# Optimization experiments

Measured on AMD Instinct MI355X. Metric: run time of the kernel, lower is better.

## Reference

```python
import jax, jax.numpy as jnp
import numpy as np

N_NODES = 20000; N_EDGES = 320000; B = 128; T = 200
EMB = 128; GH = 64; HEADS = 4; LH = 128; NSP = 64; TD = 4

def gat_conv(x, src, dst, W, att_src, att_dst, bias, heads, ch, concat):
    # PyG GATConv (eval mode, dropout off): per-edge attention + segment softmax over dst
    n = x.shape[0]
    h = (x @ W).reshape(n, heads, ch)                      # [N,H,C]
    a_s = (h * att_src[None]).sum(-1)                      # [N,H]
    a_d = (h * att_dst[None]).sum(-1)
    e = jax.nn.leaky_relu(a_s[src] + a_d[dst], 0.2)        # [E,H]
    e_max = jax.ops.segment_max(e, dst, num_segments=n)    # every node has a self-loop -> finite
    ex = jnp.exp(e - e_max[dst])
    denom = jax.ops.segment_sum(ex, dst, num_segments=n)
    alpha = ex / denom[dst]                                # [E,H]
    out = jax.ops.segment_sum(h[src] * alpha[:, :, None], dst, num_segments=n)  # [N,H,C]
    out = out.reshape(n, heads * ch) if concat else out.mean(axis=1)
    return out + bias

def lstm_dir(x, w_ih, w_hh, b):
    # single-direction LSTM, torch gate order (i, f, g, o)
    bsz = x.shape[0]
    def step(carry, xt):
        hprev, cprev = carry
        g = xt @ w_ih.T + hprev @ w_hh.T + b
        i, f, gg, o = jnp.split(g, 4, axis=-1)
        c = jax.nn.sigmoid(f) * cprev + jax.nn.sigmoid(i) * jnp.tanh(gg)
        hnew = jax.nn.sigmoid(o) * jnp.tanh(c)
        return (hnew, c), hnew
    init = (jnp.zeros((bsz, LH), x.dtype), jnp.zeros((bsz, LH), x.dtype))
    _, hs = jax.lax.scan(step, init, jnp.swapaxes(x, 0, 1))
    return jnp.swapaxes(hs, 0, 1)

def forward(x_coords, temporal_features, node_emb,
            gat1_W, gat1_att_src, gat1_att_dst, gat1_bias,
            gat2_W, gat2_att_src, gat2_att_dst, gat2_bias,
            w_ih_f, w_hh_f, b_f, w_ih_b, w_hh_b, b_b,
            attn_node_w, attn_node_b, attn_sp_w, attn_sp_b,
            fc_node_W, fc_node_b, fc_sp_W, fc_sp_b,
            edge_index, seq, lengths):
    n = x_coords.shape[0]
    node_features = jnp.concatenate([x_coords, node_emb, temporal_features], axis=1)  # [N,134]
    loops = jnp.arange(n)                                  # PyG GATConv add_self_loops=True
    src = jnp.concatenate([edge_index[0], loops])
    dst = jnp.concatenate([edge_index[1], loops])
    z = jax.nn.elu(gat_conv(node_features, src, dst, gat1_W, gat1_att_src, gat1_att_dst, gat1_bias, HEADS, GH, True))
    z = gat_conv(z, src, dst, gat2_W, gat2_att_src, gat2_att_dst, gat2_bias, 1, EMB, False)
    seq_emb = z[seq]                                       # [B,T,EMB]
    out_f = lstm_dir(seq_emb, w_ih_f, w_hh_f, b_f)
    # backward direction of packed BiLSTM: reverse each sequence within its true length
    rev_idx = jnp.clip(lengths[:, None] - 1 - jnp.arange(T)[None, :], 0, T - 1)
    x_rev = jnp.take_along_axis(seq_emb, rev_idx[:, :, None], axis=1)
    out_b = jnp.take_along_axis(lstm_dir(x_rev, w_ih_b, w_hh_b, b_b), rev_idx[:, :, None], axis=1)
    lstm_out = jnp.concatenate([out_f, out_b], axis=-1)    # [B,T,2*LH]
    mask = jnp.arange(T)[None, :] < lengths[:, None]
    def attnpool(w, bias):
        scores = jnp.where(mask, lstm_out @ w + bias, -jnp.inf)
        aw = jax.nn.softmax(scores, axis=1)
        return jnp.einsum('bt,bth->bh', aw, lstm_out)
    ctx_n = attnpool(attn_node_w, attn_node_b)
    ctx_s = attnpool(attn_sp_w, attn_sp_b)
    return (ctx_n @ fc_node_W + fc_node_b, ctx_s @ fc_sp_W + fc_sp_b)

def setup_inputs() -> dict:
    key = jax.random.key(0)
    ks = jax.random.split(key, 24)
    f = lambda i, shape, s=0.05: jax.random.normal(ks[i], shape, jnp.float32) * s
    return dict(
        x_coords=f(0, (N_NODES, 2), 1.0),
        temporal_features=f(1, (N_NODES, TD), 1.0),
        node_emb=f(2, (N_NODES, EMB)),
        gat1_W=f(3, (2 + EMB + TD, HEADS * GH)),
        gat1_att_src=f(4, (HEADS, GH)),
        gat1_att_dst=f(5, (HEADS, GH)),
        gat1_bias=jnp.zeros((HEADS * GH,), jnp.float32),
        gat2_W=f(6, (HEADS * GH, EMB)),
        gat2_att_src=f(7, (1, EMB)),
        gat2_att_dst=f(8, (1, EMB)),
        gat2_bias=jnp.zeros((EMB,), jnp.float32),
        w_ih_f=f(9, (4 * LH, EMB)), w_hh_f=f(10, (4 * LH, LH)), b_f=jnp.zeros((4 * LH,), jnp.float32),
        w_ih_b=f(11, (4 * LH, EMB)), w_hh_b=f(12, (4 * LH, LH)), b_b=jnp.zeros((4 * LH,), jnp.float32),
        attn_node_w=f(13, (2 * LH,)), attn_node_b=jnp.zeros((1,), jnp.float32),
        attn_sp_w=f(14, (2 * LH,)), attn_sp_b=jnp.zeros((1,), jnp.float32),
        fc_node_W=f(15, (2 * LH, N_NODES)), fc_node_b=jnp.zeros((N_NODES,), jnp.float32),
        fc_sp_W=f(16, (2 * LH, NSP)), fc_sp_b=jnp.zeros((NSP,), jnp.float32),
        edge_index=jax.random.randint(ks[17], (2, N_EDGES), 0, N_NODES),
        seq=jax.random.randint(ks[18], (B, T), 0, N_NODES),
        lengths=jax.random.randint(ks[19], (B,), 1, T + 1),
    )

def reference(x_coords, temporal_features, node_emb,
              gat1_W, gat1_att_src, gat1_att_dst, gat1_bias,
              gat2_W, gat2_att_src, gat2_att_dst, gat2_bias,
              w_ih_f, w_hh_f, b_f, w_ih_b, w_hh_b, b_b,
              attn_node_w, attn_node_b, attn_sp_w, attn_sp_b,
              fc_node_W, fc_node_b, fc_sp_W, fc_sp_b,
              edge_index, seq, lengths):
    return forward(x_coords, temporal_features, node_emb,
                   gat1_W, gat1_att_src, gat1_att_dst, gat1_bias,
                   gat2_W, gat2_att_src, gat2_att_dst, gat2_bias,
                   w_ih_f, w_hh_f, b_f, w_ih_b, w_hh_b, b_b,
                   attn_node_w, attn_node_b, attn_sp_w, attn_sp_b,
                   fc_node_W, fc_node_b, fc_sp_W, fc_sp_b,
                   edge_index, seq, lengths)
```

## Files before the change

### kernel.cpp

```cpp
#include <hip/hip_runtime.h>
#include <cstdint>
#include <cstddef>

#define N_NODES 20000
#define N_EDGES 320000
#define NE_TOT  (N_EDGES + N_NODES)
#define BB 128
#define TT 200
#define EMB 128
#define GH 64
#define HEADS 4
#define LH 128
#define NSP 64
#define KF 136

__global__ void k_count(const int* __restrict__ ei, int* __restrict__ cnt) {
    int e = blockIdx.x * blockDim.x + threadIdx.x;
    if (e >= NE_TOT) return;
    int d = (e < N_EDGES) ? ei[N_EDGES + e] : (e - N_EDGES);
    atomicAdd(&cnt[d], 1);
}

__global__ __launch_bounds__(1024) void k_scan(const int* __restrict__ cnt, int* __restrict__ rs) {
    __shared__ int sd[1024];
    __shared__ int carry_s;
    int tid = threadIdx.x;
    if (tid == 0) carry_s = 0;
    __syncthreads();
    for (int base = 0; base < N_NODES; base += 1024) {
        int v = (base + tid < N_NODES) ? cnt[base + tid] : 0;
        int x = v;
        sd[tid] = x;
        __syncthreads();
        for (int off = 1; off < 1024; off <<= 1) {
            int t = (tid >= off) ? sd[tid - off] : 0;
            __syncthreads();
            x += t; sd[tid] = x;
            __syncthreads();
        }
        int carry = carry_s;
        if (base + tid < N_NODES) rs[base + tid] = carry + x - v;
        __syncthreads();
        if (tid == 0) carry_s = carry + sd[1023];
        __syncthreads();
    }
    if (tid == 0) rs[N_NODES] = carry_s;
}

__global__ void k_scatter(const int* __restrict__ ei, int* __restrict__ cursor, int* __restrict__ csr) {
    int e = blockIdx.x * blockDim.x + threadIdx.x;
    if (e >= NE_TOT) return;
    int s, d;
    if (e < N_EDGES) { s = ei[e]; d = ei[N_EDGES + e]; }
    else             { s = d = e - N_EDGES; }
    int pos = atomicAdd(&cursor[d], 1);
    csr[pos] = s;
}

__global__ void k_build_nf(const float* __restrict__ xc, const float* __restrict__ tf,
                           const float* __restrict__ ne, float* __restrict__ nf) {
    int n = blockIdx.x, j = threadIdx.x;
    if (j >= KF) return;
    float v = 0.f;
    if (j < 2)        v = xc[n * 2 + j];
    else if (j < 130) v = ne[n * 128 + (j - 2)];
    else if (j < 134) v = tf[n * 4 + (j - 130)];
    nf[(size_t)n * KF + j] = v;
}

__global__ void k_build_w1p(const float* __restrict__ W, float* __restrict__ Wp) {
    int k = blockIdx.x, n = threadIdx.x;
    Wp[k * 256 + n] = (k < 134) ? W[k * 256 + n] : 0.f;
}

__global__ void k_transpose_cat(const float* __restrict__ W, float* __restrict__ WT, int colOff) {
    int idx = blockIdx.x * blockDim.x + threadIdx.x;
    if (idx >= 512 * 128) return;
    int g = idx & 511, k = idx >> 9;
    WT[k * 1024 + colOff + g] = W[g * 128 + k];
}

__global__ void k_build_bcat(const float* __restrict__ bf, const float* __restrict__ bb,
                             float* __restrict__ bcat) {
    int t = threadIdx.x;
    bcat[t] = bf[t];
    bcat[512 + t] = bb[t];
}

__global__ void k_len_prefix(const int* __restrict__ lengths, int* __restrict__ loff) {
    if (threadIdx.x == 0) {
        int acc = 0;
        for (int b = 0; b < BB; b++) { loff[b] = acc; acc += lengths[b]; }
        loff[BB] = acc;
    }
}

__global__ void k_build_rowmap(const int* __restrict__ lengths, const int* __restrict__ loff,
                               const int* __restrict__ seq, int* __restrict__ rowsrc,
                               int* __restrict__ rowdst) {
    int idx = blockIdx.x * blockDim.x + threadIdx.x;
    if (idx >= BB * TT) return;
    int b = idx / TT, t = idx - b * TT;
    if (t >= lengths[b]) return;
    int pos = loff[b] + t;
    rowsrc[pos] = seq[idx];
    rowdst[pos] = idx;
}

__global__ __launch_bounds__(256) void k_gemm_f32(
    const float* __restrict__ A, const float* __restrict__ B, float* __restrict__ C,
    int M, int N, int K, const int* __restrict__ gather, const float* __restrict__ bias)
{
    __shared__ float As[8][68];
    __shared__ float Bs[8][68];
    int tid = threadIdx.x;
    int bm = blockIdx.y << 6, bn = blockIdx.x << 6;
    int tm = (tid >> 4) << 2, tn = (tid & 15) << 2;
    float acc[4][4] = {};
    for (int k0 = 0; k0 < K; k0 += 8) {
        if (tid < 128) {
            int m = tid >> 1, kq = (tid & 1) << 2;
            int gm = bm + m;
            float4 v = make_float4(0.f, 0.f, 0.f, 0.f);
            if (gm < M) {
                int row = gather ? gather[gm] : gm;
                v = *(const float4*)(A + (size_t)row * K + k0 + kq);
            }
            As[kq + 0][m] = v.x; As[kq + 1][m] = v.y;
            As[kq + 2][m] = v.z; As[kq + 3][m] = v.w;
        } else {
            int t2 = tid - 128;
            int kk = t2 >> 4, n4 = (t2 & 15) << 2;
            int gn = bn + n4;
            float4 v = make_float4(0.f, 0.f, 0.f, 0.f);
            const float* brow = B + (size_t)(k0 + kk) * N;
            if (gn + 3 < N) v = *(const float4*)(brow + gn);
            else {
                if (gn + 0 < N) v.x = brow[gn + 0];
                if (gn + 1 < N) v.y = brow[gn + 1];
                if (gn + 2 < N) v.z = brow[gn + 2];
                if (gn + 3 < N) v.w = brow[gn + 3];
            }
            *(float4*)(&Bs[kk][n4]) = v;
        }
        __syncthreads();
#pragma unroll
        for (int k = 0; k < 8; k++) {
            float4 av = *(const float4*)&As[k][tm];
            float4 bv = *(const float4*)&Bs[k][tn];
            acc[0][0] += av.x * bv.x; acc[0][1] += av.x * bv.y; acc[0][2] += av.x * bv.z; acc[0][3] += av.x * bv.w;
            acc[1][0] += av.y * bv.x; acc[1][1] += av.y * bv.y; acc[1][2] += av.y * bv.z; acc[1][3] += av.y * bv.w;
            acc[2][0] += av.z * bv.x; acc[2][1] += av.z * bv.y; acc[2][2] += av.z * bv.z; acc[2][3] += av.z * bv.w;
            acc[3][0] += av.w * bv.x; acc[3][1] += av.w * bv.y; acc[3][2] += av.w * bv.z; acc[3][3] += av.w * bv.w;
        }
        __syncthreads();
    }
#pragma unroll
    for (int i = 0; i < 4; i++) {
        int gm = bm + tm + i;
        if (gm >= M) continue;
#pragma unroll
        for (int j = 0; j < 4; j++) {
            int gn = bn + tn + j;
            if (gn >= N) continue;
            float r = acc[i][j];
            if (bias) r += bias[gn];
            C[(size_t)gm * N + gn] = r;
        }
    }
}

__global__ __launch_bounds__(256) void k_gemm_f32_rs(
    const float* __restrict__ A, const float* __restrict__ B, float* __restrict__ C,
    const int* __restrict__ Mdev, int N, int K,
    const int* __restrict__ rowsrc, const int* __restrict__ rowdst,
    const float* __restrict__ bias)
{
    int M = Mdev[BB];
    int bm = blockIdx.y << 6, bn = blockIdx.x << 6;
    if (bm >= M) return;
    __shared__ float As[8][68];
    __shared__ float Bs[8][68];
    int tid = threadIdx.x;
    int tm = (tid >> 4) << 2, tn = (tid & 15) << 2;
    float acc[4][4] = {};
    for (int k0 = 0; k0 < K; k0 += 8) {
        if (tid < 128) {
            int m = tid >> 1, kq = (tid & 1) << 2;
            int gm = bm + m;
            float4 v = make_float4(0.f, 0.f, 0.f, 0.f);
            if (gm < M) {
                int row = rowsrc[gm];
                v = *(const float4*)(A + (size_t)row * K + k0 + kq);
            }
            As[kq + 0][m] = v.x; As[kq + 1][m] = v.y;
            As[kq + 2][m] = v.z; As[kq + 3][m] = v.w;
        } else {
            int t2 = tid - 128;
            int kk = t2 >> 4, n4 = (t2 & 15) << 2;
            int gn = bn + n4;
            const float* brow = B + (size_t)(k0 + kk) * N;
            *(float4*)(&Bs[kk][n4]) = *(const float4*)(brow + gn);
        }
        __syncthreads();
#pragma unroll
        for (int k = 0; k < 8; k++) {
            float4 av = *(const float4*)&As[k][tm];
            float4 bv = *(const float4*)&Bs[k][tn];
            acc[0][0] += av.x * bv.x; acc[0][1] += av.x * bv.y; acc[0][2] += av.x * bv.z; acc[0][3] += av.x * bv.w;
            acc[1][0] += av.y * bv.x; acc[1][1] += av.y * bv.y; acc[1][2] += av.y * bv.z; acc[1][3] += av.y * bv.w;
            acc[2][0] += av.z * bv.x; acc[2][1] += av.z * bv.y; acc[2][2] += av.z * bv.z; acc[2][3] += av.z * bv.w;
            acc[3][0] += av.w * bv.x; acc[3][1] += av.w * bv.y; acc[3][2] += av.w * bv.z; acc[3][3] += av.w * bv.w;
        }
        __syncthreads();
    }
#pragma unroll
    for (int i = 0; i < 4; i++) {
        int gm = bm + tm + i;
        if (gm >= M) continue;
        size_t crow = (size_t)rowdst[gm] * N;
#pragma unroll
        for (int j = 0; j < 4; j++) {
            int gn = bn + tn + j;
            float r = acc[i][j] + bias[gn];
            C[crow + gn] = r;
        }
    }
}

template <int H, int C>
__global__ void k_attn_dots(const float* __restrict__ hm, const float* __restrict__ asrc,
                            const float* __restrict__ adst, float* __restrict__ a_s,
                            float* __restrict__ a_d) {
    int wave = (blockIdx.x * blockDim.x + threadIdx.x) >> 6;
    int lane = threadIdx.x & 63;
    if (wave >= N_NODES * H) return;
    int n = wave / H, h = wave - n * H;
    const float* row = hm + (size_t)n * (H * C) + h * C;
    float ps = 0.f, pd = 0.f;
#pragma unroll
    for (int c0 = 0; c0 < C; c0 += 64) {
        float v = row[c0 + lane];
        ps += v * asrc[h * C + c0 + lane];
        pd += v * adst[h * C + c0 + lane];
    }
#pragma unroll
    for (int off = 32; off > 0; off >>= 1) {
        ps += __shfl_down(ps, off);
        pd += __shfl_down(pd, off);
    }
    if (lane == 0) { a_s[wave] = ps; a_d[wave] = pd; }
}

template <int H, int C, bool DO_ELU>
__global__ void k_gat_aggregate(const float* __restrict__ hm, const float* __restrict__ a_s,
                                const float* __restrict__ a_d, const int* __restrict__ rs,
                                const int* __restrict__ csr, const float* __restrict__ bias,
                                float* __restrict__ out) {
    int d = blockIdx.x;
    int tid = threadIdx.x;
    int h = tid / C;
    int r0 = rs[d], r1 = rs[d + 1];
    float adv = a_d[d * H + h];
    float m = -1e30f;
    for (int j = r0; j < r1; j++) {
        int s = csr[j];
        float e = a_s[s * H + h] + adv;
        e = (e > 0.f) ? e : 0.2f * e;
        m = fmaxf(m, e);
    }
    float den = 0.f, acc = 0.f;
    for (int j = r0; j < r1; j++) {
        int s = csr[j];
        float e = a_s[s * H + h] + adv;
        e = (e > 0.f) ? e : 0.2f * e;
        float ex = __expf(e - m);
        den += ex;
        acc += ex * hm[(size_t)s * (H * C) + tid];
    }
    float r = acc / den + bias[tid];
    if (DO_ELU) r = (r > 0.f) ? r : expm1f(r);
    out[(size_t)d * (H * C) + tid] = r;
}

__device__ __forceinline__ float sigmf(float x) { return 1.f / (1.f + __expf(-x)); }
__device__ __forceinline__ float tanhfast(float x) {
    x = fminf(fmaxf(x, -20.f), 20.f);
    float e = __expf(2.f * x);
    return (e - 1.f) / (e + 1.f);
}

__global__ __launch_bounds__(512, 2) void k_lstm(
    const float* __restrict__ xgcat,
    const float* __restrict__ whh_f, const float* __restrict__ whh_b,
    const int* __restrict__ lengths, float* __restrict__ lstm_out)
{
    int b = blockIdx.x & 127;
    int dir = blockIdx.x >> 7;
    int tid = threadIdx.x;
    int u = tid & 127;
    int j = tid >> 7;
    const float* whh = dir ? whh_b : whh_f;
    const float* xg = xgcat + (dir << 9);
    int L = lengths[b];
    float4 w4[4][8];
#pragma unroll
    for (int m = 0; m < 4; m++) {
        const float4* wrow = (const float4*)(whh + (size_t)(m * LH + u) * LH + j * 32);
#pragma unroll
        for (int q = 0; q < 8; q++) w4[m][q] = wrow[q];
    }
    __shared__ float hbuf[LH];
    __shared__ float pbuf[4][4 * LH];
    if (tid < LH) hbuf[tid] = 0.f;
    float c = 0.f;
    float hv = 0.f;
    float x0 = 0.f, x1 = 0.f, x2 = 0.f, x3 = 0.f;
    if (j == 0) {
        int tx0 = dir ? (L - 1) : 0;
        const float* xrow = xg + ((size_t)(b * TT + tx0) << 10);
        x0 = xrow[u]; x1 = xrow[LH + u]; x2 = xrow[2 * LH + u]; x3 = xrow[3 * LH + u];
    }
    __syncthreads();
    for (int t = 0; t < L; t++) {
        if (j == 0 && t > 0) {
            int txp = dir ? (L - t) : (t - 1);
            lstm_out[((size_t)b * TT + txp) * (2 * LH) + dir * LH + u] = hv;
        }
        float x0n = 0.f, x1n = 0.f, x2n = 0.f, x3n = 0.f;
        if (j == 0 && t + 1 < L) {
            int tx1 = dir ? (L - 2 - t) : (t + 1);
            const float* xrow = xg + ((size_t)(b * TT + tx1) << 10);
            x0n = xrow[u]; x1n = xrow[LH + u]; x2n = xrow[2 * LH + u]; x3n = xrow[3 * LH + u];
        }
        const float4* hp = (const float4*)(hbuf + j * 32);
        float4 h[8];
#pragma unroll
        for (int q = 0; q < 8; q++) h[q] = hp[q];
        float a0 = x0, a1 = x1, a2 = x2, a3 = x3;
#pragma unroll
        for (int q = 0; q < 8; q++) {
            float4 hq = h[q];
            a0 += w4[0][q].x * hq.x + w4[0][q].y * hq.y + w4[0][q].z * hq.z + w4[0][q].w * hq.w;
            a1 += w4[1][q].x * hq.x + w4[1][q].y * hq.y + w4[1][q].z * hq.z + w4[1][q].w * hq.w;
            a2 += w4[2][q].x * hq.x + w4[2][q].y * hq.y + w4[2][q].z * hq.z + w4[2][q].w * hq.w;
            a3 += w4[3][q].x * hq.x + w4[3][q].y * hq.y + w4[3][q].z * hq.z + w4[3][q].w * hq.w;
        }
        pbuf[j][0 * LH + u] = a0;
        pbuf[j][1 * LH + u] = a1;
        pbuf[j][2 * LH + u] = a2;
        pbuf[j][3 * LH + u] = a3;
        asm volatile("s_waitcnt lgkmcnt(0)" ::: "memory");
        __builtin_amdgcn_sched_barrier(0);
        __builtin_amdgcn_s_barrier();
        if (tid < LH) {
            float gi = (pbuf[0][0 * LH + u] + pbuf[1][0 * LH + u]) + (pbuf[2][0 * LH + u] + pbuf[3][0 * LH + u]);
            float gf = (pbuf[0][1 * LH + u] + pbuf[1][1 * LH + u]) + (pbuf[2][1 * LH + u] + pbuf[3][1 * LH + u]);
            float gG = (pbuf[0][2 * LH + u] + pbuf[1][2 * LH + u]) + (pbuf[2][2 * LH + u] + pbuf[3][2 * LH + u]);
            float go = (pbuf[0][3 * LH + u] + pbuf[1][3 * LH + u]) + (pbuf[2][3 * LH + u] + pbuf[3][3 * LH + u]);
            float ig = sigmf(gi);
            float fg = sigmf(gf);
            float gg = tanhfast(gG);
            float og = sigmf(go);
            c = fg * c + ig * gg;
            hv = og * tanhfast(c);
            hbuf[u] = hv;
        }
        asm volatile("s_waitcnt lgkmcnt(0)" ::: "memory");
        __builtin_amdgcn_sched_barrier(0);
        __builtin_amdgcn_s_barrier();
        x0 = x0n; x1 = x1n; x2 = x2n; x3 = x3n;
    }
    if (j == 0) {
        int txp = dir ? 0 : (L - 1);
        lstm_out[((size_t)b * TT + txp) * (2 * LH) + dir * LH + u] = hv;
    }
}

__global__ __launch_bounds__(256) void k_attnpool(
    const float* __restrict__ lo, const int* __restrict__ lengths,
    const float* __restrict__ wn, const float* __restrict__ bn,
    const float* __restrict__ wsp, const float* __restrict__ bsp,
    float* __restrict__ ctxn, float* __restrict__ ctxs)
{
    int b = blockIdx.x;
    int tid = threadIdx.x;
    int L = lengths[b];
    __shared__ float sn[TT], ss[TT];
    __shared__ float red[256];
    int wv = tid >> 6, lane = tid & 63;
    for (int t = wv; t < L; t += 4) {
        const float* row = lo + ((size_t)b * TT + t) * (2 * LH);
        float pn = 0.f, ps = 0.f;
#pragma unroll
        for (int c0 = 0; c0 < 256; c0 += 64) {
            float v = row[c0 + lane];
            pn += v * wn[c0 + lane];
            ps += v * wsp[c0 + lane];
        }
#pragma unroll
        for (int off = 32; off > 0; off >>= 1) {
            pn += __shfl_down(pn, off);
            ps += __shfl_down(ps, off);
        }
        if (lane == 0) { sn[t] = pn + bn[0]; ss[t] = ps + bsp[0]; }
    }
    __syncthreads();
    float vn = (tid < L) ? sn[tid] : -1e30f;
    float vs = (tid < L) ? ss[tid] : -1e30f;
    red[tid] = vn; __syncthreads();
    for (int s = 128; s > 0; s >>= 1) { if (tid < s) red[tid] = fmaxf(red[tid], red[tid + s]); __syncthreads(); }
    float mn = red[0]; __syncthreads();
    red[tid] = vs; __syncthreads();
    for (int s = 128; s > 0; s >>= 1) { if (tid < s) red[tid] = fmaxf(red[tid], red[tid + s]); __syncthreads(); }
    float ms = red[0]; __syncthreads();
    float en = (tid < L) ? __expf(vn - mn) : 0.f;
    float es = (tid < L) ? __expf(vs - ms) : 0.f;
    red[tid] = en; __syncthreads();
    for (int s = 128; s > 0; s >>= 1) { if (tid < s) red[tid] += red[tid + s]; __syncthreads(); }
    float dn = red[0]; __syncthreads();
    red[tid] = es; __syncthreads();
    for (int s = 128; s > 0; s >>= 1) { if (tid < s) red[tid] += red[tid + s]; __syncthreads(); }
    float dsum = red[0]; __syncthreads();
    if (tid < L) { sn[tid] = en / dn; ss[tid] = es / dsum; }
    __syncthreads();
    float an = 0.f, asv = 0.f;
    for (int t = 0; t < L; t++) {
        float v = lo[((size_t)b * TT + t) * (2 * LH) + tid];
        an += sn[t] * v;
        asv += ss[t] * v;
    }
    ctxn[b * (2 * LH) + tid] = an;
    ctxs[b * (2 * LH) + tid] = asv;
}

extern "C" void kernel_launch(void* const* d_in, const int* in_sizes, int n_in,
                              void* d_out, int out_size, void* d_ws, size_t ws_size,
                              hipStream_t stream) {
    (void)in_sizes; (void)n_in; (void)out_size; (void)ws_size;
    const float* x_coords = (const float*)d_in[0];
    const float* temporal = (const float*)d_in[1];
    const float* node_emb = (const float*)d_in[2];
    const float* gat1_W   = (const float*)d_in[3];
    const float* gat1_as  = (const float*)d_in[4];
    const float* gat1_ad  = (const float*)d_in[5];
    const float* gat1_b   = (const float*)d_in[6];
    const float* gat2_W   = (const float*)d_in[7];
    const float* gat2_as  = (const float*)d_in[8];
    const float* gat2_ad  = (const float*)d_in[9];
    const float* gat2_b   = (const float*)d_in[10];
    const float* w_ih_f   = (const float*)d_in[11];
    const float* w_hh_f   = (const float*)d_in[12];
    const float* b_f      = (const float*)d_in[13];
    const float* w_ih_b   = (const float*)d_in[14];
    const float* w_hh_b   = (const float*)d_in[15];
    const float* b_b      = (const float*)d_in[16];
    const float* attn_n_w = (const float*)d_in[17];
    const float* attn_n_b = (const float*)d_in[18];
    const float* attn_s_w = (const float*)d_in[19];
    const float* attn_s_b = (const float*)d_in[20];
    const float* fc_n_W   = (const float*)d_in[21];
    const float* fc_n_b   = (const float*)d_in[22];
    const float* fc_s_W   = (const float*)d_in[23];
    const float* fc_s_b   = (const float*)d_in[24];
    const int*   edge_idx = (const int*)d_in[25];
    const int*   seq      = (const int*)d_in[26];
    const int*   lengths  = (const int*)d_in[27];

    char* ws = (char*)d_ws;
    size_t off = 0;
    auto alloc = [&](size_t bytes) -> char* {
        char* p = ws + off;
        off += (bytes + 255) & ~(size_t)255;
        return p;
    };
    int*   cnt      = (int*)alloc((size_t)N_NODES * 4);
    int*   rowstart = (int*)alloc((size_t)(N_NODES + 1) * 4);
    int*   cursor   = (int*)alloc((size_t)N_NODES * 4);
    int*   csr      = (int*)alloc((size_t)NE_TOT * 4);
    float* z2       = (float*)alloc((size_t)N_NODES * EMB * 4);
    float* lstm_o   = (float*)alloc((size_t)BB * TT * 2 * LH * 4);
    float* ctxn     = (float*)alloc((size_t)BB * 2 * LH * 4);
    float* ctxs     = (float*)alloc((size_t)BB * 2 * LH * 4);
    float* wTcat    = (float*)alloc((size_t)128 * 1024 * 4);
    float* bcat     = (float*)alloc((size_t)1024 * 4);
    int*   loff     = (int*)alloc((size_t)(BB + 1) * 4);
    int*   rowsrc   = (int*)alloc((size_t)BB * TT * 4);
    int*   rowdst   = (int*)alloc((size_t)BB * TT * 4);
    float* nf  = (float*)(ws + off);
    float* w1p = nf + (size_t)N_NODES * KF;
    float* h1  = w1p + (size_t)KF * 256;
    float* as1 = h1 + (size_t)N_NODES * 256;
    float* ad1 = as1 + (size_t)N_NODES * 4;
    float* z1  = ad1 + (size_t)N_NODES * 4;
    float* h2  = z1 + (size_t)N_NODES * 256;
    float* as2 = h2 + (size_t)N_NODES * 128;
    float* ad2 = as2 + (size_t)N_NODES;
    float* xgcat = (float*)(ws + off);

    hipMemsetAsync(cnt, 0, (size_t)N_NODES * 4, stream);
    k_count<<<(NE_TOT + 255) / 256, 256, 0, stream>>>(edge_idx, cnt);
    k_scan<<<1, 1024, 0, stream>>>(cnt, rowstart);
    hipMemcpyAsync(cursor, rowstart, (size_t)N_NODES * 4, hipMemcpyDeviceToDevice, stream);
    k_scatter<<<(NE_TOT + 255) / 256, 256, 0, stream>>>(edge_idx, cursor, csr);

    k_len_prefix<<<1, 64, 0, stream>>>(lengths, loff);
    k_build_rowmap<<<(BB * TT + 255) / 256, 256, 0, stream>>>(lengths, loff, seq, rowsrc, rowdst);

    k_build_nf<<<N_NODES, 192, 0, stream>>>(x_coords, temporal, node_emb, nf);
    k_build_w1p<<<KF, 256, 0, stream>>>(gat1_W, w1p);
    {
        dim3 g(4, (N_NODES + 63) / 64);
        k_gemm_f32<<<g, 256, 0, stream>>>(nf, w1p, h1, N_NODES, 256, KF, nullptr, nullptr);
    }
    k_attn_dots<HEADS, GH><<<(N_NODES * HEADS + 3) / 4, 256, 0, stream>>>(h1, gat1_as, gat1_ad, as1, ad1);
    k_gat_aggregate<HEADS, GH, true><<<N_NODES, 256, 0, stream>>>(h1, as1, ad1, rowstart, csr, gat1_b, z1);

    {
        dim3 g(2, (N_NODES + 63) / 64);
        k_gemm_f32<<<g, 256, 0, stream>>>(z1, gat2_W, h2, N_NODES, 128, 256, nullptr, nullptr);
    }
    k_attn_dots<1, EMB><<<(N_NODES + 3) / 4, 256, 0, stream>>>(h2, gat2_as, gat2_ad, as2, ad2);
    k_gat_aggregate<1, EMB, false><<<N_NODES, 128, 0, stream>>>(h2, as2, ad2, rowstart, csr, gat2_b, z2);

    k_transpose_cat<<<(512 * 128 + 255) / 256, 256, 0, stream>>>(w_ih_f, wTcat, 0);
    k_transpose_cat<<<(512 * 128 + 255) / 256, 256, 0, stream>>>(w_ih_b, wTcat, 512);
    k_build_bcat<<<1, 512, 0, stream>>>(b_f, b_b, bcat);
    {
        dim3 g(1024 / 64, (BB * TT + 63) / 64);
        k_gemm_f32_rs<<<g, 256, 0, stream>>>(z2, wTcat, xgcat, loff, 1024, 128, rowsrc, rowdst, bcat);
    }

    k_lstm<<<256, 512, 0, stream>>>(xgcat, w_hh_f, w_hh_b, lengths, lstm_o);

    k_attnpool<<<BB, 256, 0, stream>>>(lstm_o, lengths, attn_n_w, attn_n_b, attn_s_w, attn_s_b, ctxn, ctxs);

    float* out_node = (float*)d_out;
    float* out_sp   = out_node + (size_t)BB * N_NODES;
    {
        dim3 g((N_NODES + 63) / 64, 2);
        k_gemm_f32<<<g, 256, 0, stream>>>(ctxn, fc_n_W, out_node, BB, N_NODES, 256, nullptr, fc_n_b);
    }
    {
        dim3 g(1, 2);
        k_gemm_f32<<<g, 256, 0, stream>>>(ctxs, fc_s_W, out_sp, BB, NSP, 256, nullptr, fc_s_b);
    }
}
```

Before: 791.5 us.

## Reduce LSTM gate partial sums with DPP lane shuffles and double-buffer hidden state

Result: no change. 800.6 us (+1.2%).

```diff
diff --git a/kernel.cpp b/kernel.cpp
--- a/kernel.cpp
+++ b/kernel.cpp
@@ -290,6 +290,15 @@
     return (e - 1.f) / (e + 1.f);
 }
 
+__device__ __forceinline__ float dpp_add_x1(float x) {
+    int y = __builtin_amdgcn_update_dpp(0, __float_as_int(x), 0xB1, 0xF, 0xF, true);
+    return x + __int_as_float(y);
+}
+__device__ __forceinline__ float dpp_add_x2(float x) {
+    int y = __builtin_amdgcn_update_dpp(0, __float_as_int(x), 0x4E, 0xF, 0xF, true);
+    return x + __int_as_float(y);
+}
+
 __global__ __launch_bounds__(512, 2) void k_lstm(
     const float* __restrict__ xgcat,
     const float* __restrict__ whh_f, const float* __restrict__ whh_b,
@@ -298,46 +307,48 @@
     int b = blockIdx.x & 127;
     int dir = blockIdx.x >> 7;
     int tid = threadIdx.x;
-    int u = tid & 127;
-    int j = tid >> 7;
+    int wv = tid >> 6;
+    int lane = tid & 63;
+    int kp = lane & 3;
+    int ul = lane >> 2;
+    int u = (wv << 4) + ul;
     const float* whh = dir ? whh_b : whh_f;
     const float* xg = xgcat + (dir << 9);
     int L = lengths[b];
     float4 w4[4][8];
 #pragma unroll
     for (int m = 0; m < 4; m++) {
-        const float4* wrow = (const float4*)(whh + (size_t)(m * LH + u) * LH + j * 32);
+        const float4* wrow = (const float4*)(whh + (size_t)(m * LH + u) * LH + kp * 32);
 #pragma unroll
         for (int q = 0; q < 8; q++) w4[m][q] = wrow[q];
     }
-    __shared__ float hbuf[LH];
-    __shared__ float pbuf[4][4 * LH];
-    if (tid < LH) hbuf[tid] = 0.f;
-    float c = 0.f;
-    float hv = 0.f;
+    __shared__ __align__(16) float hbuf[2][160];
+    if (tid < LH) hbuf[0][(tid >> 5) * 40 + (tid & 31)] = 0.f;
+    float c = 0.f, hv = 0.f;
+    const bool act = (kp == 0);
     float x0 = 0.f, x1 = 0.f, x2 = 0.f, x3 = 0.f;
-    if (j == 0) {
+    if (act) {
         int tx0 = dir ? (L - 1) : 0;
         const float* xrow = xg + ((size_t)(b * TT + tx0) << 10);
         x0 = xrow[u]; x1 = xrow[LH + u]; x2 = xrow[2 * LH + u]; x3 = xrow[3 * LH + u];
     }
     __syncthreads();
     for (int t = 0; t < L; t++) {
-        if (j == 0 && t > 0) {
+        if (act && t > 0) {
             int txp = dir ? (L - t) : (t - 1);
             lstm_out[((size_t)b * TT + txp) * (2 * LH) + dir * LH + u] = hv;
         }
         float x0n = 0.f, x1n = 0.f, x2n = 0.f, x3n = 0.f;
-        if (j == 0 && t + 1 < L) {
+        if (act && t + 1 < L) {
             int tx1 = dir ? (L - 2 - t) : (t + 1);
             const float* xrow = xg + ((size_t)(b * TT + tx1) << 10);
             x0n = xrow[u]; x1n = xrow[LH + u]; x2n = xrow[2 * LH + u]; x3n = xrow[3 * LH + u];
         }
-        const float4* hp = (const float4*)(hbuf + j * 32);
+        const float4* hp = (const float4*)(&hbuf[t & 1][kp * 40]);
         float4 h[8];
 #pragma unroll
         for (int q = 0; q < 8; q++) h[q] = hp[q];
-        float a0 = x0, a1 = x1, a2 = x2, a3 = x3;
+        float a0 = 0.f, a1 = 0.f, a2 = 0.f, a3 = 0.f;
 #pragma unroll
         for (int q = 0; q < 8; q++) {
             float4 hq = h[q];
@@ -346,32 +357,25 @@
             a2 += w4[2][q].x * hq.x + w4[2][q].y * hq.y + w4[2][q].z * hq.z + w4[2][q].w * hq.w;
             a3 += w4[3][q].x * hq.x + w4[3][q].y * hq.y + w4[3][q].z * hq.z + w4[3][q].w * hq.w;
         }
-        pbuf[j][0 * LH + u] = a0;
-        pbuf[j][1 * LH + u] = a1;
-        pbuf[j][2 * LH + u] = a2;
-        pbuf[j][3 * LH + u] = a3;
-        asm volatile("s_waitcnt lgkmcnt(0)" ::: "memory");
-        __builtin_amdgcn_sched_barrier(0);
-        __builtin_amdgcn_s_barrier();
-        if (tid < LH) {
-            float gi = (pbuf[0][0 * LH + u] + pbuf[1][0 * LH + u]) + (pbuf[2][0 * LH + u] + pbuf[3][0 * LH + u]);
-            float gf = (pbuf[0][1 * LH + u] + pbuf[1][1 * LH + u]) + (pbuf[2][1 * LH + u] + pbuf[3][1 * LH + u]);
-            float gG = (pbuf[0][2 * LH + u] + pbuf[1][2 * LH + u]) + (pbuf[2][2 * LH + u] + pbuf[3][2 * LH + u]);
-            float go = (pbuf[0][3 * LH + u] + pbuf[1][3 * LH + u]) + (pbuf[2][3 * LH + u] + pbuf[3][3 * LH + u]);
-            float ig = sigmf(gi);
-            float fg = sigmf(gf);
-            float gg = tanhfast(gG);
-            float og = sigmf(go);
+        a0 = dpp_add_x2(dpp_add_x1(a0));
+        a1 = dpp_add_x2(dpp_add_x1(a1));
+        a2 = dpp_add_x2(dpp_add_x1(a2));
+        a3 = dpp_add_x2(dpp_add_x1(a3));
+        if (act) {
+            float ig = sigmf(a0 + x0);
+            float fg = sigmf(a1 + x1);
+            float gg = tanhfast(a2 + x2);
+            float og = sigmf(a3 + x3);
             c = fg * c + ig * gg;
             hv = og * tanhfast(c);
-            hbuf[u] = hv;
+            hbuf[(t + 1) & 1][(u >> 5) * 40 + (u & 31)] = hv;
         }
         asm volatile("s_waitcnt lgkmcnt(0)" ::: "memory");
         __builtin_amdgcn_sched_barrier(0);
         __builtin_amdgcn_s_barrier();
         x0 = x0n; x1 = x1n; x2 = x2n; x3 = x3n;
     }
-    if (j == 0) {
+    if (act) {
         int txp = dir ? 0 : (L - 1);
         lstm_out[((size_t)b * TT + txp) * (2 * LH) + dir * LH + u] = hv;
     }
```

## Fuse attention dots into GEMM epilogue and merge small prep kernels

Applied to the files above, without the earlier changes.

After: 744.2 us. 1.06x faster.

```diff
diff --git a/kernel.cpp b/kernel.cpp
--- a/kernel.cpp
+++ b/kernel.cpp
@@ -21,30 +21,38 @@
     atomicAdd(&cnt[d], 1);
 }
 
-__global__ __launch_bounds__(1024) void k_scan(const int* __restrict__ cnt, int* __restrict__ rs) {
+__global__ __launch_bounds__(1024) void k_scan(const int* __restrict__ cnt,
+                                               int* __restrict__ rs,
+                                               int* __restrict__ cursor) {
     __shared__ int sd[1024];
-    __shared__ int carry_s;
     int tid = threadIdx.x;
-    if (tid == 0) carry_s = 0;
+    const int EPT = 20;
+    int base = tid * EPT;
+    int v[EPT];
+    int s = 0;
+#pragma unroll
+    for (int i = 0; i < EPT; i++) {
+        int idx = base + i;
+        v[i] = (idx < N_NODES) ? cnt[idx] : 0;
+        s += v[i];
+    }
+    int x = s;
+    sd[tid] = x;
     __syncthreads();
-    for (int base = 0; base < N_NODES; base += 1024) {
-        int v = (base + tid < N_NODES) ? cnt[base + tid] : 0;
-        int x = v;
-        sd[tid] = x;
-        __syncthreads();
-        for (int off = 1; off < 1024; off <<= 1) {
-            int t = (tid >= off) ? sd[tid - off] : 0;
-            __syncthreads();
-            x += t; sd[tid] = x;
-            __syncthreads();
-        }
-        int carry = carry_s;
-        if (base + tid < N_NODES) rs[base + tid] = carry + x - v;
-        __syncthreads();
-        if (tid == 0) carry_s = carry + sd[1023];
-        __syncthreads();
-    }
-    if (tid == 0) rs[N_NODES] = carry_s;
+    for (int off = 1; off < 1024; off <<= 1) {
+        int t = (tid >= off) ? sd[tid - off] : 0;
+        __syncthreads();
+        x += t; sd[tid] = x;
+        __syncthreads();
+    }
+    int run = x - s;
+#pragma unroll
+    for (int i = 0; i < EPT; i++) {
+        int idx = base + i;
+        if (idx < N_NODES) { rs[idx] = run; cursor[idx] = run; }
+        run += v[i];
+    }
+    if (tid == 1023) rs[N_NODES] = x;
 }
 
 __global__ void k_scatter(const int* __restrict__ ei, int* __restrict__ cursor, int* __restrict__ csr) {
@@ -57,59 +65,65 @@
     csr[pos] = s;
 }
 
-__global__ void k_build_nf(const float* __restrict__ xc, const float* __restrict__ tf,
-                           const float* __restrict__ ne, float* __restrict__ nf) {
-    int n = blockIdx.x, j = threadIdx.x;
-    if (j >= KF) return;
-    float v = 0.f;
-    if (j < 2)        v = xc[n * 2 + j];
-    else if (j < 130) v = ne[n * 128 + (j - 2)];
-    else if (j < 134) v = tf[n * 4 + (j - 130)];
-    nf[(size_t)n * KF + j] = v;
-}
-
-__global__ void k_build_w1p(const float* __restrict__ W, float* __restrict__ Wp) {
-    int k = blockIdx.x, n = threadIdx.x;
-    Wp[k * 256 + n] = (k < 134) ? W[k * 256 + n] : 0.f;
-}
-
-__global__ void k_transpose_cat(const float* __restrict__ W, float* __restrict__ WT, int colOff) {
-    int idx = blockIdx.x * blockDim.x + threadIdx.x;
-    if (idx >= 512 * 128) return;
-    int g = idx & 511, k = idx >> 9;
-    WT[k * 1024 + colOff + g] = W[g * 128 + k];
-}
-
-__global__ void k_build_bcat(const float* __restrict__ bf, const float* __restrict__ bb,
-                             float* __restrict__ bcat) {
-    int t = threadIdx.x;
-    bcat[t] = bf[t];
-    bcat[512 + t] = bb[t];
-}
-
-__global__ void k_len_prefix(const int* __restrict__ lengths, int* __restrict__ loff) {
-    if (threadIdx.x == 0) {
-        int acc = 0;
-        for (int b = 0; b < BB; b++) { loff[b] = acc; acc += lengths[b]; }
-        loff[BB] = acc;
-    }
-}
-
-__global__ void k_build_rowmap(const int* __restrict__ lengths, const int* __restrict__ loff,
-                               const int* __restrict__ seq, int* __restrict__ rowsrc,
-                               int* __restrict__ rowdst) {
+__global__ void k_build_rowmap(const int* __restrict__ lengths, const int* __restrict__ seq,
+                               int* __restrict__ rowsrc, int* __restrict__ rowdst,
+                               int* __restrict__ loff) {
     int idx = blockIdx.x * blockDim.x + threadIdx.x;
     if (idx >= BB * TT) return;
     int b = idx / TT, t = idx - b * TT;
+    int base = 0;
+    for (int i = 0; i < BB; i++) base += (i < b) ? lengths[i] : 0;
+    if (idx == 0) {
+        int tot = 0;
+        for (int i = 0; i < BB; i++) tot += lengths[i];
+        loff[BB] = tot;
+    }
     if (t >= lengths[b]) return;
-    int pos = loff[b] + t;
+    int pos = base + t;
     rowsrc[pos] = seq[idx];
     rowdst[pos] = idx;
 }
 
+__global__ void k_prep1(const float* __restrict__ xc, const float* __restrict__ tf,
+                        const float* __restrict__ ne, const float* __restrict__ W,
+                        float* __restrict__ nf, float* __restrict__ Wp) {
+    if (blockIdx.x < N_NODES) {
+        int n = blockIdx.x, j = threadIdx.x;
+        if (j >= KF) return;
+        float v = 0.f;
+        if (j < 2)        v = xc[n * 2 + j];
+        else if (j < 130) v = ne[n * 128 + (j - 2)];
+        else if (j < 134) v = tf[n * 4 + (j - 130)];
+        nf[(size_t)n * KF + j] = v;
+    } else {
+        int k = blockIdx.x - N_NODES, n = threadIdx.x;
+        Wp[k * 256 + n] = (k < 134) ? W[k * 256 + n] : 0.f;
+    }
+}
+
+__global__ void k_prep2(const float* __restrict__ wf, const float* __restrict__ wb,
+                        const float* __restrict__ bf, const float* __restrict__ bb,
+                        float* __restrict__ WT, float* __restrict__ bcat) {
+    int idx = blockIdx.x * blockDim.x + threadIdx.x;
+    if (idx < 512 * 128) {
+        int g = idx & 511, k = idx >> 9;
+        WT[k * 1024 + g] = wf[g * 128 + k];
+    } else if (idx < 2 * 512 * 128) {
+        int j = idx - 512 * 128;
+        int g = j & 511, k = j >> 9;
+        WT[k * 1024 + 512 + g] = wb[g * 128 + k];
+    } else if (idx < 2 * 512 * 128 + 512) {
+        int t = idx - 2 * 512 * 128;
+        bcat[t] = bf[t];
+        bcat[512 + t] = bb[t];
+    }
+}
+
 __global__ __launch_bounds__(256) void k_gemm_f32(
     const float* __restrict__ A, const float* __restrict__ B, float* __restrict__ C,
-    int M, int N, int K, const int* __restrict__ gather, const float* __restrict__ bias)
+    int M, int N, int K, const int* __restrict__ gather, const float* __restrict__ bias,
+    const float* __restrict__ asrc, const float* __restrict__ adst,
+    float* __restrict__ a_s, float* __restrict__ a_d, int AC)
 {
     __shared__ float As[8][68];
     __shared__ float Bs[8][68];
@@ -168,6 +182,29 @@
             C[(size_t)gm * N + gn] = r;
         }
     }
+    if (asrc) {
+        int H = N / AC;
+        int h = bn / AC;
+#pragma unroll
+        for (int i = 0; i < 4; i++) {
+            int gm = bm + tm + i;
+            float ps = 0.f, pd = 0.f;
+#pragma unroll
+            for (int j = 0; j < 4; j++) {
+                int gn = bn + tn + j;
+                ps += acc[i][j] * asrc[gn];
+                pd += acc[i][j] * adst[gn];
+            }
+            for (int off = 8; off >= 1; off >>= 1) {
+                ps += __shfl_down(ps, off);
+                pd += __shfl_down(pd, off);
+            }
+            if ((tid & 15) == 0 && gm < M) {
+                atomicAdd(&a_s[gm * H + h], ps);
+                atomicAdd(&a_d[gm * H + h], pd);
+            }
+        }
+    }
 }
 
 __global__ __launch_bounds__(256) void k_gemm_f32_rs(
@@ -228,28 +265,68 @@
     }
 }
 
-template <int H, int C>
-__global__ void k_attn_dots(const float* __restrict__ hm, const float* __restrict__ asrc,
-                            const float* __restrict__ adst, float* __restrict__ a_s,
-                            float* __restrict__ a_d) {
-    int wave = (blockIdx.x * blockDim.x + threadIdx.x) >> 6;
-    int lane = threadIdx.x & 63;
-    if (wave >= N_NODES * H) return;
-    int n = wave / H, h = wave - n * H;
-    const float* row = hm + (size_t)n * (H * C) + h * C;
-    float ps = 0.f, pd = 0.f;
-#pragma unroll
-    for (int c0 = 0; c0 < C; c0 += 64) {
-        float v = row[c0 + lane];
-        ps += v * asrc[h * C + c0 + lane];
-        pd += v * adst[h * C + c0 + lane];
-    }
-#pragma unroll
-    for (int off = 32; off > 0; off >>= 1) {
-        ps += __shfl_down(ps, off);
-        pd += __shfl_down(pd, off);
-    }
-    if (lane == 0) { a_s[wave] = ps; a_d[wave] = pd; }
+__global__ __launch_bounds__(256) void k_gemm_heads(
+    const float* __restrict__ ctxn, const float* __restrict__ ctxs,
+    const float* __restrict__ Wn, const float* __restrict__ bnod,
+    const float* __restrict__ Wsp, const float* __restrict__ bsp,
+    float* __restrict__ outn, float* __restrict__ outs)
+{
+    const float* A; const float* B; float* C; const float* bias; int N; int bn;
+    if (blockIdx.x < 313) { A = ctxn; B = Wn;  C = outn; bias = bnod; N = N_NODES; bn = blockIdx.x << 6; }
+    else                  { A = ctxs; B = Wsp; C = outs; bias = bsp;  N = NSP;     bn = 0; }
+    const int M = BB, K = 2 * LH;
+    __shared__ float As[8][68];
+    __shared__ float Bs[8][68];
+    int tid = threadIdx.x;
+    int bm = blockIdx.y << 6;
+    int tm = (tid >> 4) << 2, tn = (tid & 15) << 2;
+    float acc[4][4] = {};
+    for (int k0 = 0; k0 < K; k0 += 8) {
+        if (tid < 128) {
+            int m = tid >> 1, kq = (tid & 1) << 2;
+            int gm = bm + m;
+            float4 v = make_float4(0.f, 0.f, 0.f, 0.f);
+            if (gm < M) v = *(const float4*)(A + (size_t)gm * K + k0 + kq);
+            As[kq + 0][m] = v.x; As[kq + 1][m] = v.y;
+            As[kq + 2][m] = v.z; As[kq + 3][m] = v.w;
+        } else {
+            int t2 = tid - 128;
+            int kk = t2 >> 4, n4 = (t2 & 15) << 2;
+            int gn = bn + n4;
+            float4 v = make_float4(0.f, 0.f, 0.f, 0.f);
+            const float* brow = B + (size_t)(k0 + kk) * N;
+            if (gn + 3 < N) v = *(const float4*)(brow + gn);
+            else {
+                if (gn + 0 < N) v.x = brow[gn + 0];
+                if (gn + 1 < N) v.y = brow[gn + 1];
+                if (gn + 2 < N) v.z = brow[gn + 2];
+                if (gn + 3 < N) v.w = brow[gn + 3];
+            }
+            *(float4*)(&Bs[kk][n4]) = v;
+        }
+        __syncthreads();
+#pragma unroll
+        for (int k = 0; k < 8; k++) {
+            float4 av = *(const float4*)&As[k][tm];
+            float4 bv = *(const float4*)&Bs[k][tn];
+            acc[0][0] += av.x * bv.x; acc[0][1] += av.x * bv.y; acc[0][2] += av.x * bv.z; acc[0][3] += av.x * bv.w;
+            acc[1][0] += av.y * bv.x; acc[1][1] += av.y * bv.y; acc[1][2] += av.y * bv.z; acc[1][3] += av.y * bv.w;
+            acc[2][0] += av.z * bv.x; acc[2][1] += av.z * bv.y; acc[2][2] += av.z * bv.z; acc[2][3] += av.z * bv.w;
+            acc[3][0] += av.w * bv.x; acc[3][1] += av.w * bv.y; acc[3][2] += av.w * bv.z; acc[3][3] += av.w * bv.w;
+        }
+        __syncthreads();
+    }
+#pragma unroll
+    for (int i = 0; i < 4; i++) {
+        int gm = bm + tm + i;
+        if (gm >= M) continue;
+#pragma unroll
+        for (int j = 0; j < 4; j++) {
+            int gn = bn + tn + j;
+            if (gn >= N) continue;
+            C[(size_t)gm * N + gn] = acc[i][j] + bias[gn];
+        }
+    }
 }
 
 template <int H, int C, bool DO_ELU>
@@ -475,6 +552,11 @@
         return p;
     };
     int*   cnt      = (int*)alloc((size_t)N_NODES * 4);
+    float* as1      = (float*)alloc((size_t)N_NODES * 4 * 4);
+    float* ad1      = (float*)alloc((size_t)N_NODES * 4 * 4);
+    float* as2      = (float*)alloc((size_t)N_NODES * 4);
+    float* ad2      = (float*)alloc((size_t)N_NODES * 4);
+    size_t zero_end = off;
     int*   rowstart = (int*)alloc((size_t)(N_NODES + 1) * 4);
     int*   cursor   = (int*)alloc((size_t)N_NODES * 4);
     int*   csr      = (int*)alloc((size_t)NE_TOT * 4);
@@ -490,59 +572,39 @@
     float* nf  = (float*)(ws + off);
     float* w1p = nf + (size_t)N_NODES * KF;
     float* h1  = w1p + (size_t)KF * 256;
-    float* as1 = h1 + (size_t)N_NODES * 256;
-    float* ad1 = as1 + (size_t)N_NODES * 4;
-    float* z1  = ad1 + (size_t)N_NODES * 4;
+    float* z1  = h1 + (size_t)N_NODES * 256;
     float* h2  = z1 + (size_t)N_NODES * 256;
-    float* as2 = h2 + (size_t)N_NODES * 128;
-    float* ad2 = as2 + (size_t)N_NODES;
     float* xgcat = (float*)(ws + off);
 
-    hipMemsetAsync(cnt, 0, (size_t)N_NODES * 4, stream);
+    hipMemsetAsync(cnt, 0, zero_end, stream);
     k_count<<<(NE_TOT + 255) / 256, 256, 0, stream>>>(edge_idx, cnt);
-    k_scan<<<1, 1024, 0, stream>>>(cnt, rowstart);
-    hipMemcpyAsync(cursor, rowstart, (size_t)N_NODES * 4, hipMemcpyDeviceToDevice, stream);
+    k_scan<<<1, 1024, 0, stream>>>(cnt, rowstart, cursor);
     k_scatter<<<(NE_TOT + 255) / 256, 256, 0, stream>>>(edge_idx, cursor, csr);
-
-    k_len_prefix<<<1, 64, 0, stream>>>(lengths, loff);
-    k_build_rowmap<<<(BB * TT + 255) / 256, 256, 0, stream>>>(lengths, loff, seq, rowsrc, rowdst);
-
-    k_build_nf<<<N_NODES, 192, 0, stream>>>(x_coords, temporal, node_emb, nf);
-    k_build_w1p<<<KF, 256, 0, stream>>>(gat1_W, w1p);
+    k_build_rowmap<<<(BB * TT + 255) / 256, 256, 0, stream>>>(lengths, seq, rowsrc, rowdst, loff);
+    k_prep1<<<N_NODES + KF, 256, 0, stream>>>(x_coords, temporal, node_emb, gat1_W, nf, w1p);
     {
         dim3 g(4, (N_NODES + 63) / 64);
-        k_gemm_f32<<<g, 256, 0, stream>>>(nf, w1p, h1, N_NODES, 256, KF, nullptr, nullptr);
-    }
-    k_attn_dots<HEADS, GH><<<(N_NODES * HEADS + 3) / 4, 256, 0, stream>>>(h1, gat1_as, gat1_ad, as1, ad1);
+        k_gemm_f32<<<g, 256, 0, stream>>>(nf, w1p, h1, N_NODES, 256, KF, nullptr, nullptr,
+                                          gat1_as, gat1_ad, as1, ad1, GH);
+    }
     k_gat_aggregate<HEADS, GH, true><<<N_NODES, 256, 0, stream>>>(h1, as1, ad1, rowstart, csr, gat1_b, z1);
-
     {
         dim3 g(2, (N_NODES + 63) / 64);
-        k_gemm_f32<<<g, 256, 0, stream>>>(z1, gat2_W, h2, N_NODES, 128, 256, nullptr, nullptr);
-    }
-    k_attn_dots<1, EMB><<<(N_NODES + 3) / 4, 256, 0, stream>>>(h2, gat2_as, gat2_ad, as2, ad2);
+        k_gemm_f32<<<g, 256, 0, stream>>>(z1, gat2_W, h2, N_NODES, 128, 256, nullptr, nullptr,
+                                          gat2_as, gat2_ad, as2, ad2, EMB);
+    }
     k_gat_aggregate<1, EMB, false><<<N_NODES, 128, 0, stream>>>(h2, as2, ad2, rowstart, csr, gat2_b, z2);
-
-    k_transpose_cat<<<(512 * 128 + 255) / 256, 256, 0, stream>>>(w_ih_f, wTcat, 0);
-    k_transpose_cat<<<(512 * 128 + 255) / 256, 256, 0, stream>>>(w_ih_b, wTcat, 512);
-    k_build_bcat<<<1, 512, 0, stream>>>(b_f, b_b, bcat);
+    k_prep2<<<(2 * 512 * 128 + 512 + 255) / 256, 256, 0, stream>>>(w_ih_f, w_ih_b, b_f, b_b, wTcat, bcat);
     {
         dim3 g(1024 / 64, (BB * TT + 63) / 64);
         k_gemm_f32_rs<<<g, 256, 0, stream>>>(z2, wTcat, xgcat, loff, 1024, 128, rowsrc, rowdst, bcat);
     }
-
     k_lstm<<<256, 512, 0, stream>>>(xgcat, w_hh_f, w_hh_b, lengths, lstm_o);
-
     k_attnpool<<<BB, 256, 0, stream>>>(lstm_o, lengths, attn_n_w, attn_n_b, attn_s_w, attn_s_b, ctxn, ctxs);
-
     float* out_node = (float*)d_out;
     float* out_sp   = out_node + (size_t)BB * N_NODES;
     {
-        dim3 g((N_NODES + 63) / 64, 2);
-        k_gemm_f32<<<g, 256, 0, stream>>>(ctxn, fc_n_W, out_node, BB, N_NODES, 256, nullptr, fc_n_b);
-    }
-    {
-        dim3 g(1, 2);
-        k_gemm_f32<<<g, 256, 0, stream>>>(ctxs, fc_s_W, out_sp, BB, NSP, 256, nullptr, fc_s_b);
-    }
-}
+        dim3 g(314, 2);
+        k_gemm_heads<<<g, 256, 0, stream>>>(ctxn, ctxs, fc_n_W, fc_n_b, fc_s_W, fc_s_b, out_node, out_sp);
+    }
+}
```
